# Kernel tuning notes

Hardware: AMD Instinct MI355X
Metric: run time of the kernel (lower is better)

## Reference

```python
import jax, jax.numpy as jnp
import numpy as np

N_M, N_C, D, H, E, EL = 200000, 50000, 128, 64, 1000000, 100000


def gat_conv(h_src, h_dst, W_src, W_dst, a_src, a_dst, b, src, dst, n_dst):
    # PyG GATConv (heads=1): project, per-edge attention logit, segment softmax over dst, weighted scatter-sum.
    hs = h_src @ W_src                      # [Ns, H]
    hd = h_dst @ W_dst                      # [Nd, H]
    al_s = hs @ a_src                       # [Ns]
    al_d = hd @ a_dst                       # [Nd]
    alpha = jax.nn.leaky_relu(al_s[src] + al_d[dst], 0.2)   # [E]
    m = jax.ops.segment_max(alpha, dst, num_segments=n_dst)
    m = jnp.where(jnp.isfinite(m), m, 0.0)
    e = jnp.exp(alpha - m[dst])
    denom = jax.ops.segment_sum(e, dst, num_segments=n_dst)
    w = e / jnp.maximum(denom[dst], 1e-16)
    out = jax.ops.segment_sum(w[:, None] * hs[src], dst, num_segments=n_dst)
    return out + b


def setup_inputs() -> dict:
    key = jax.random.key(0)
    ks = jax.random.split(key, 32)
    p = lambda k, s: (jax.random.normal(k, s, jnp.float32) * 0.1)
    inp = {
        'x_m': jax.random.normal(ks[0], (N_M, D), jnp.float32),
        'x_c': jax.random.normal(ks[1], (N_C, D), jnp.float32),
        'src_mc': jax.random.randint(ks[2], (E,), 0, N_M, jnp.int32),
        'dst_mc': jax.random.randint(ks[3], (E,), 0, N_C, jnp.int32),
        'src_cm': jax.random.randint(ks[4], (E,), 0, N_C, jnp.int32),
        'dst_cm': jax.random.randint(ks[5], (E,), 0, N_M, jnp.int32),
        'row': jax.random.randint(ks[6], (EL,), 0, N_M, jnp.int32),
        'col': jax.random.randint(ks[7], (EL,), 0, N_C, jnp.int32),
        'W1s_mc': p(ks[8], (D, H)), 'W1d_mc': p(ks[9], (D, H)),
        'a1s_mc': p(ks[10], (H,)), 'a1d_mc': p(ks[11], (H,)), 'b1_mc': p(ks[12], (H,)),
        'W1s_cm': p(ks[13], (D, H)), 'W1d_cm': p(ks[14], (D, H)),
        'a1s_cm': p(ks[15], (H,)), 'a1d_cm': p(ks[16], (H,)), 'b1_cm': p(ks[17], (H,)),
        'W2s_mc': p(ks[18], (H, H)), 'W2d_mc': p(ks[19], (H, H)),
        'a2s_mc': p(ks[20], (H,)), 'a2d_mc': p(ks[21], (H,)), 'b2_mc': p(ks[22], (H,)),
        'W2s_cm': p(ks[23], (H, H)), 'W2d_cm': p(ks[24], (H, H)),
        'a2s_cm': p(ks[25], (H,)), 'a2d_cm': p(ks[26], (H,)), 'b2_cm': p(ks[27], (H,)),
        'Wd1': p(ks[28], (2 * H, H)), 'bd1': p(ks[29], (H,)),
        'Wd2': p(ks[30], (H, 2)), 'bd2': p(ks[31], (2,)),
    }
    return inp


def reference(x_m, x_c, src_mc, dst_mc, src_cm, dst_cm, row, col,
              W1s_mc, W1d_mc, a1s_mc, a1d_mc, b1_mc,
              W1s_cm, W1d_cm, a1s_cm, a1d_cm, b1_cm,
              W2s_mc, W2d_mc, a2s_mc, a2d_mc, b2_mc,
              W2s_cm, W2d_cm, a2s_cm, a2d_cm, b2_cm,
              Wd1, bd1, Wd2, bd2):
    # Layer 1: materials receive only via concepts->materials edges; concepts via materials->concepts.
    z_c = jax.nn.relu(gat_conv(x_m, x_c, W1s_mc, W1d_mc, a1s_mc, a1d_mc, b1_mc, src_mc, dst_mc, N_C))
    z_m = jax.nn.relu(gat_conv(x_c, x_m, W1s_cm, W1d_cm, a1s_cm, a1d_cm, b1_cm, src_cm, dst_cm, N_M))
    # Layer 2 (no activation)
    z_c2 = gat_conv(z_m, z_c, W2s_mc, W2d_mc, a2s_mc, a2d_mc, b2_mc, src_mc, dst_mc, N_C)
    z_m2 = gat_conv(z_c, z_m, W2s_cm, W2d_cm, a2s_cm, a2d_cm, b2_cm, src_cm, dst_cm, N_M)
    # Edge decoder: gather-concat + 2-layer MLP (no activation between, per source)
    z = jnp.concatenate([z_m2[row], z_c2[col]], axis=-1)   # [EL, 2H]
    z = z @ Wd1 + bd1
    z = z @ Wd2 + bd2
    return z.reshape(-1)
```

## Files before the change

### kernel.cpp

```cpp
#include <hip/hip_runtime.h>
#include <hip/hip_fp16.h>
#include <cstdint>
#include <cstddef>

typedef _Float16 f16x8 __attribute__((ext_vector_type(8)));
typedef float f32x4 __attribute__((ext_vector_type(4)));

__device__ __forceinline__ float exp_am8(float a) {
    return __builtin_amdgcn_exp2f(fmaf(a, 1.442695040888963f, -11.541560327111707f));
}

__global__ __launch_bounds__(256) void bucket_hist(const int* __restrict__ dA,
                                                   int* __restrict__ bcntA, int shA,
                                                   const int* __restrict__ dB,
                                                   int* __restrict__ bcntB, int shB,
                                                   int E, int nblkA) {
    __shared__ int h[256];
    const int* dst; int* bcnt; int sh; int base;
    if ((int)blockIdx.x < nblkA) { dst = dA; bcnt = bcntA; sh = shA; base = blockIdx.x * 4096; }
    else { dst = dB; bcnt = bcntB; sh = shB; base = (blockIdx.x - nblkA) * 4096; }
    int t = threadIdx.x;
    h[t] = 0;
    __syncthreads();
#pragma unroll
    for (int j = 0; j < 16; ++j) {
        int i = base + j * 256 + t;
        if (i < E) atomicAdd(&h[dst[i] >> sh], 1);
    }
    __syncthreads();
    int c = h[t];
    if (c > 0) atomicAdd(&bcnt[t], c);
}

__global__ void bucket_scan(const int* __restrict__ bcntA, int nbkA,
                            int* __restrict__ bbaseA, int* __restrict__ bcurA,
                            int* __restrict__ offA, int nA,
                            const int* __restrict__ bcntB, int nbkB,
                            int* __restrict__ bbaseB, int* __restrict__ bcurB,
                            int* __restrict__ offB, int nB, int E) {
    int t = threadIdx.x;
    if (t == 0) {
        int run = 0;
        for (int i = 0; i < nbkA; ++i) { bbaseA[i] = run; bcurA[i] = run; run += bcntA[i]; }
        bbaseA[nbkA] = run;
        offA[nA] = E;
    }
    if (t == 64) {
        int run = 0;
        for (int i = 0; i < nbkB; ++i) { bbaseB[i] = run; bcurB[i] = run; run += bcntB[i]; }
        bbaseB[nbkB] = run;
        offB[nB] = E;
    }
}

__global__ __launch_bounds__(256) void bucket_scatter(
    const int* __restrict__ srcA, const int* __restrict__ dstA,
    int* __restrict__ bcurA, unsigned* __restrict__ pairsA,
    const int* __restrict__ srcB, const int* __restrict__ dstB,
    int* __restrict__ bcurB, unsigned* __restrict__ pairsB,
    int E, int nblkA, int shA, int shB, int srcbits) {
    __shared__ int bcnt[256];
    __shared__ int bbase[256];
    const int* src; const int* dst; int* bcur; unsigned* pairs; int sh; int base;
    if ((int)blockIdx.x < nblkA) {
        src = srcA; dst = dstA; bcur = bcurA; pairs = pairsA; sh = shA;
        base = blockIdx.x * 4096;
    } else {
        src = srcB; dst = dstB; bcur = bcurB; pairs = pairsB; sh = shB;
        base = (blockIdx.x - nblkA) * 4096;
    }
    int t = threadIdx.x;
    int msk = (1 << sh) - 1;
    bcnt[t] = 0;
    __syncthreads();
    int sreg[16], dreg[16];
#pragma unroll
    for (int j = 0; j < 16; ++j) {
        int i = base + j * 256 + t;
        if (i < E) {
            sreg[j] = src[i];
            dreg[j] = dst[i];
            atomicAdd(&bcnt[dreg[j] >> sh], 1);
        } else {
            dreg[j] = -1;
        }
    }
    __syncthreads();
    {
        int c = bcnt[t];
        int g = (c > 0) ? atomicAdd(&bcur[t], c) : 0;
        bbase[t] = g;
        bcnt[t] = 0;
    }
    __syncthreads();
#pragma unroll
    for (int j = 0; j < 16; ++j) {
        if (dreg[j] >= 0) {
            int b = dreg[j] >> sh;
            int r = atomicAdd(&bcnt[b], 1);
            pairs[bbase[b] + r] = ((unsigned)(dreg[j] & msk) << srcbits) | (unsigned)sreg[j];
        }
    }
}

__global__ __launch_bounds__(256) void bucket_expand2(
    const unsigned* __restrict__ pairsA, const int* __restrict__ bbaseA, int nA,
    int* __restrict__ offA, int* __restrict__ csrA, int shA, int nbA,
    const unsigned* __restrict__ pairsB, const int* __restrict__ bbaseB, int nB,
    int* __restrict__ offB, int* __restrict__ csrB, int shB, int srcbits) {
    __shared__ int lcnt[1024];
    __shared__ int red[256];
    const unsigned* pairs; const int* bbase; int n; int* off; int* csr; int sh; int b;
    if ((int)blockIdx.x < nbA) {
        pairs = pairsA; bbase = bbaseA; n = nA; off = offA; csr = csrA; sh = shA;
        b = blockIdx.x;
    } else {
        pairs = pairsB; bbase = bbaseB; n = nB; off = offB; csr = csrB; sh = shB;
        b = blockIdx.x - nbA;
    }
    int dpb = 1 << sh;
    int d0 = b << sh;
    int t = threadIdx.x;
    unsigned smask = (1u << srcbits) - 1u;
    for (int dl = t; dl < dpb; dl += 256) lcnt[dl] = 0;
    __syncthreads();
    int pbeg = bbase[b], pend = bbase[b + 1];
    for (int i = pbeg + t; i < pend; i += 256)
        atomicAdd(&lcnt[pairs[i] >> srcbits], 1);
    __syncthreads();
    int per = (dpb + 255) >> 8;
    int i0 = t * per;
    int s = 0;
    for (int j = 0; j < per; ++j) {
        int dl = i0 + j;
        if (dl < dpb) s += lcnt[dl];
    }
    red[t] = s;
    __syncthreads();
    for (int st = 1; st < 256; st <<= 1) {
        int tmp = (t >= st) ? red[t - st] : 0;
        __syncthreads();
        red[t] += tmp;
        __syncthreads();
    }
    int run = pbeg + red[t] - s;
    for (int j = 0; j < per; ++j) {
        int dl = i0 + j;
        if (dl < dpb) {
            int c = lcnt[dl];
            if (d0 + dl < n) off[d0 + dl] = run;
            lcnt[dl] = run;
            run += c;
        }
    }
    __syncthreads();
    for (int i = pbeg + t; i < pend; i += 256) {
        unsigned p = pairs[i];
        int dl = (int)(p >> srcbits);
        int pos = atomicAdd(&lcnt[dl], 1);
        csr[pos] = (int)(p & smask);
    }
}

__global__ __launch_bounds__(256) void pack_w2(
    const float* __restrict__ Wa0, const float* __restrict__ Wb0, _Float16* __restrict__ P0,
    const float* __restrict__ Wa1, const float* __restrict__ Wb1, _Float16* __restrict__ P1) {
    int b = blockIdx.x;
    const float* Wa; const float* Wb; _Float16* Wp; int lb;
    if (b < 64) { Wa = Wa0; Wb = Wb0; Wp = P0; lb = b; }
    else        { Wa = Wa1; Wb = Wb1; Wp = P1; lb = b - 64; }
    constexpr int K = 128;
    constexpr int NKB = K / 32;
    int i = lb * 256 + threadIdx.x;
    if (i >= 128 * K) return;
    int k = i >> 7, c = i & 127;
    float v = (c < 64) ? Wa[k * 64 + c] : Wb[k * 64 + (c - 64)];
    int ct = c >> 4, lr = c & 15, kb = k >> 5, lk = (k & 31) >> 3, e = k & 7;
    Wp[((ct * NKB + kb) * 64 + (lr + 16 * lk)) * 8 + e] = (_Float16)v;
}

__global__ void decoder_prep3(const float* __restrict__ Wd1, const float* __restrict__ bd1,
                              const float* __restrict__ Wd2, const float* __restrict__ bd2,
                              const float* __restrict__ b2_cm, const float* __restrict__ b2_mc,
                              const float* __restrict__ W2s_mc, const float* __restrict__ a2s_mc,
                              const float* __restrict__ W2d_cm, const float* __restrict__ a2d_cm,
                              const float* __restrict__ W2s_cm, const float* __restrict__ a2s_cm,
                              const float* __restrict__ W2d_mc, const float* __restrict__ a2d_mc,
                              float* __restrict__ Wc, float* __restrict__ bc,
                              float* __restrict__ bq,
                              float4* __restrict__ foldA, float4* __restrict__ foldB) {
    __shared__ float WcS[256];
    int t = threadIdx.x;
    int k = t >> 1, c = t & 1;
    float s = 0.f;
    for (int j = 0; j < 64; ++j) s += Wd1[k * 64 + j] * Wd2[j * 2 + c];
    Wc[k * 2 + c] = s;
    WcS[k * 2 + c] = s;
    if (k == 0) {
        float b = bd2[c];
        for (int j = 0; j < 64; ++j) b += bd1[j] * Wd2[j * 2 + c];
        bc[c] = b;
    }
    __syncthreads();
    if (t < 2) {
        float v = 0.f;
        for (int j = 0; j < 64; ++j) v += b2_cm[j] * WcS[j * 2 + t];
        bq[t] = v;
    } else if (t < 4) {
        int cc = t - 2;
        float v = 0.f;
        for (int j = 0; j < 64; ++j) v += b2_mc[j] * WcS[(64 + j) * 2 + cc];
        bq[t] = v;
    }
    if (t < 64) {
        int j = t;
        float fa = 0.f, fd = 0.f, qx = 0.f, qy = 0.f;
        for (int cc = 0; cc < 64; ++cc) {
            float ws = W2s_mc[j * 64 + cc];
            fa += ws * a2s_mc[cc];
            qx += ws * WcS[(64 + cc) * 2 + 0];
            qy += ws * WcS[(64 + cc) * 2 + 1];
            fd += W2d_cm[j * 64 + cc] * a2d_cm[cc];
        }
        foldA[j] = make_float4(fa, fd, qx, qy);
    } else if (t < 128) {
        int j = t - 64;
        float fa = 0.f, fd = 0.f, qx = 0.f, qy = 0.f;
        for (int cc = 0; cc < 64; ++cc) {
            float ws = W2s_cm[j * 64 + cc];
            fa += ws * a2s_cm[cc];
            qx += ws * WcS[cc * 2 + 0];
            qy += ws * WcS[cc * 2 + 1];
            fd += W2d_mc[j * 64 + cc] * a2d_mc[cc];
        }
        foldB[j] = make_float4(fa, fd, qx, qy);
    }
}

template <int K>
__global__ __launch_bounds__(256) void proj_mfma3_kernel(const float* __restrict__ X, int N,
                                                         const _Float16* __restrict__ Wp,
                                                         const float* __restrict__ a0v,
                                                         const float* __restrict__ a1v,
                                                         __half* __restrict__ out0,
                                                         float* __restrict__ al0,
                                                         float* __restrict__ al1) {
    constexpr int NKB = K / 32;
    __shared__ __align__(16) _Float16 Wlds[128 * K];
    int t = threadIdx.x;
    constexpr int NV = (128 * K) / 8;
#pragma unroll
    for (int i = t; i < NV; i += 256)
        ((uint4*)Wlds)[i] = ((const uint4*)Wp)[i];
    __syncthreads();

    int rt = blockIdx.x * 64;
    int wv = t >> 6, lane = t & 63, lr = lane & 15, lk = lane >> 4;
    int row = rt + wv * 16 + lr;
    int rowc = row < N ? row : N - 1;

    f32x4 acc[8];
#pragma unroll
    for (int i = 0; i < 8; ++i) acc[i] = f32x4{0.f, 0.f, 0.f, 0.f};

    const f16x8* Wf = (const f16x8*)Wlds;
#pragma unroll
    for (int kb = 0; kb < NKB; ++kb) {
        f16x8 bf;
        const float* xr = X + (size_t)rowc * K + kb * 32 + lk * 8;
        float4 x0 = *(const float4*)xr;
        float4 x1 = *(const float4*)(xr + 4);
        bf[0] = (_Float16)x0.x; bf[1] = (_Float16)x0.y;
        bf[2] = (_Float16)x0.z; bf[3] = (_Float16)x0.w;
        bf[4] = (_Float16)x1.x; bf[5] = (_Float16)x1.y;
        bf[6] = (_Float16)x1.z; bf[7] = (_Float16)x1.w;
#pragma unroll
        for (int ct = 0; ct < 8; ++ct) {
            acc[ct] = __builtin_amdgcn_mfma_f32_16x16x32_f16(Wf[(ct * NKB + kb) * 64 + lane],
                                                             bf, acc[ct], 0, 0, 0);
        }
    }

    float p0 = 0.f, p1 = 0.f;
#pragma unroll
    for (int ct = 0; ct < 4; ++ct) {
        float4 aq = ((const float4*)a0v)[ct * 4 + lk];
        f32x4 v = acc[ct];
        p0 += v[0] * aq.x + v[1] * aq.y + v[2] * aq.z + v[3] * aq.w;
    }
#pragma unroll
    for (int ct = 0; ct < 4; ++ct) {
        float4 aq = ((const float4*)a1v)[ct * 4 + lk];
        f32x4 v = acc[4 + ct];
        p1 += v[0] * aq.x + v[1] * aq.y + v[2] * aq.z + v[3] * aq.w;
    }
    p0 += __shfl_xor(p0, 16); p0 += __shfl_xor(p0, 32);
    p1 += __shfl_xor(p1, 16); p1 += __shfl_xor(p1, 32);
    if (row < N) {
#pragma unroll
        for (int ct = 0; ct < 4; ++ct) {
            f32x4 v = acc[ct];
            __half2 h01 = __floats2half2_rn(v[0], v[1]);
            __half2 h23 = __floats2half2_rn(v[2], v[3]);
            uint2 pk;
            pk.x = *(const unsigned int*)&h01;
            pk.y = *(const unsigned int*)&h23;
            *(uint2*)(out0 + ((size_t)row << 6) + ct * 16 + lk * 4) = pk;
        }
        if (lane < 16) { al0[row] = p0; al1[row] = p1; }
    }
}

#define AGG_CAP 64
#define AGG_PAD 66

__global__ __launch_bounds__(256) void gat_aggregate9f(
    const int* __restrict__ off0, const int* __restrict__ csr0,
    const __half* __restrict__ hs0, const float* __restrict__ als0,
    const float* __restrict__ ald0, const float* __restrict__ bias0,
    const float4* __restrict__ fold0, float* __restrict__ als2_0,
    float* __restrict__ ald2_0, float2* __restrict__ q2_0, int n0,
    const int* __restrict__ off1, const int* __restrict__ csr1,
    const __half* __restrict__ hs1, const float* __restrict__ als1,
    const float* __restrict__ ald1, const float* __restrict__ bias1,
    const float4* __restrict__ fold1, float* __restrict__ als2_1,
    float* __restrict__ ald2_1, float2* __restrict__ q2_1, int n1,
    int nb0) {
    __shared__ uint2 wP[16][AGG_PAD];
    int t = threadIdx.x;
    int slot = t >> 4;
    int sub = t & 15;

    const int* off; const int* csr; const __half* hs; const float* als;
    const float* ald; const float* bias; const float4* fold;
    float* als2; float* ald2; float2* q2; int nd; int b;
    if (blockIdx.x < (unsigned)nb0) {
        b = blockIdx.x;
        off = off0; csr = csr0; hs = hs0; als = als0; ald = ald0; bias = bias0;
        fold = fold0; als2 = als2_0; ald2 = ald2_0; q2 = q2_0; nd = n0;
    } else {
        b = blockIdx.x - nb0;
        off = off1; csr = csr1; hs = hs1; als = als1; ald = ald1; bias = bias1;
        fold = fold1; als2 = als2_1; ald2 = ald2_1; q2 = q2_1; nd = n1;
    }
    int d = b * 16 + slot;
    bool active = d < nd;
    int beg = 0, deg = 0;
    float aldv = 0.f;
    if (active) {
        beg = off[d];
        deg = off[d + 1] - beg;
        aldv = ald[d];
    }
    float4 bl4 = ((const float4*)bias)[sub];
    uint2* WP = wP[slot];

    float sum = 0.f;
    for (int i = sub; i < deg; i += 16) {
        int s = csr[beg + i];
        float a = als[s] + aldv;
        a = (a >= 0.f) ? a : 0.2f * a;
        float w = exp_am8(a);
        sum += w;
        if (i < AGG_CAP) {
            __half hw = __float2half_rn(w);
            __half2 h2 = __half2half2(hw);
            WP[i] = make_uint2(*(const unsigned int*)&h2, (unsigned int)s);
        }
    }
    sum += __shfl_xor(sum, 1);
    sum += __shfl_xor(sum, 2);
    sum += __shfl_xor(sum, 4);
    sum += __shfl_xor(sum, 8);
    float inv = 1.f / fmaxf(sum, 1e-16f);

    int dc = deg < AGG_CAP ? deg : AGG_CAP;
    const uint2* hs4 = (const uint2*)hs;
    __half2 z = __floats2half2_rn(0.f, 0.f);
    __half2 aA = z, aB = z, aC = z, aD = z;
    int i = 0;
    for (; i + 8 <= dc; i += 8) {
        uint4 q0 = *(const uint4*)&WP[i];
        uint4 q1 = *(const uint4*)&WP[i + 2];
        uint4 q2r = *(const uint4*)&WP[i + 4];
        uint4 q3 = *(const uint4*)&WP[i + 6];
        uint2 v0 = hs4[(size_t)q0.y * 16 + sub];
        uint2 v1 = hs4[(size_t)q0.w * 16 + sub];
        uint2 v2 = hs4[(size_t)q1.y * 16 + sub];
        uint2 v3 = hs4[(size_t)q1.w * 16 + sub];
        uint2 v4 = hs4[(size_t)q2r.y * 16 + sub];
        uint2 v5 = hs4[(size_t)q2r.w * 16 + sub];
        uint2 v6 = hs4[(size_t)q3.y * 16 + sub];
        uint2 v7 = hs4[(size_t)q3.w * 16 + sub];
        aA = __hfma2(*(const __half2*)&q0.x, *(const __half2*)&v0.x, aA);
        aB = __hfma2(*(const __half2*)&q0.x, *(const __half2*)&v0.y, aB);
        aC = __hfma2(*(const __half2*)&q0.z, *(const __half2*)&v1.x, aC);
        aD = __hfma2(*(const __half2*)&q0.z, *(const __half2*)&v1.y, aD);
        aA = __hfma2(*(const __half2*)&q1.x, *(const __half2*)&v2.x, aA);
        aB = __hfma2(*(const __half2*)&q1.x, *(const __half2*)&v2.y, aB);
        aC = __hfma2(*(const __half2*)&q1.z, *(const __half2*)&v3.x, aC);
        aD = __hfma2(*(const __half2*)&q1.z, *(const __half2*)&v3.y, aD);
        aA = __hfma2(*(const __half2*)&q2r.x, *(const __half2*)&v4.x, aA);
        aB = __hfma2(*(const __half2*)&q2r.x, *(const __half2*)&v4.y, aB);
        aC = __hfma2(*(const __half2*)&q2r.z, *(const __half2*)&v5.x, aC);
        aD = __hfma2(*(const __half2*)&q2r.z, *(const __half2*)&v5.y, aD);
        aA = __hfma2(*(const __half2*)&q3.x, *(const __half2*)&v6.x, aA);
        aB = __hfma2(*(const __half2*)&q3.x, *(const __half2*)&v6.y, aB);
        aC = __hfma2(*(const __half2*)&q3.z, *(const __half2*)&v7.x, aC);
        aD = __hfma2(*(const __half2*)&q3.z, *(const __half2*)&v7.y, aD);
    }
    for (; i + 2 <= dc; i += 2) {
        uint4 q = *(const uint4*)&WP[i];
        uint2 v0 = hs4[(size_t)q.y * 16 + sub];
        uint2 v1 = hs4[(size_t)q.w * 16 + sub];
        aA = __hfma2(*(const __half2*)&q.x, *(const __half2*)&v0.x, aA);
        aB = __hfma2(*(const __half2*)&q.x, *(const __half2*)&v0.y, aB);
        aC = __hfma2(*(const __half2*)&q.z, *(const __half2*)&v1.x, aC);
        aD = __hfma2(*(const __half2*)&q.z, *(const __half2*)&v1.y, aD);
    }
    if (i < dc) {
        uint2 u = WP[i];
        uint2 v = hs4[(size_t)u.y * 16 + sub];
        aA = __hfma2(*(const __half2*)&u.x, *(const __half2*)&v.x, aA);
        aB = __hfma2(*(const __half2*)&u.x, *(const __half2*)&v.y, aB);
    }
    for (int j = AGG_CAP; j < deg; ++j) {
        int s = csr[beg + j];
        float a = als[s] + aldv;
        a = (a >= 0.f) ? a : 0.2f * a;
        __half hw = __float2half_rn(exp_am8(a));
        __half2 w2 = __half2half2(hw);
        uint2 v = hs4[(size_t)s * 16 + sub];
        aA = __hfma2(w2, *(const __half2*)&v.x, aA);
        aB = __hfma2(w2, *(const __half2*)&v.y, aB);
    }
    float2 fA = __half22float2(aA);
    float2 fB = __half22float2(aB);
    float2 fC = __half22float2(aC);
    float2 fD = __half22float2(aD);
    float o0 = (fA.x + fC.x) * inv + bl4.x;
    float o1 = (fA.y + fC.y) * inv + bl4.y;
    float o2 = (fB.x + fD.x) * inv + bl4.z;
    float o3 = (fB.y + fD.y) * inv + bl4.w;
    if (deg == 0) { o0 = bl4.x; o1 = bl4.y; o2 = bl4.z; o3 = bl4.w; }
    o0 = fmaxf(o0, 0.f); o1 = fmaxf(o1, 0.f);
    o2 = fmaxf(o2, 0.f); o3 = fmaxf(o3, 0.f);

    float4 f0 = fold[4 * sub + 0];
    float4 f1 = fold[4 * sub + 1];
    float4 f2 = fold[4 * sub + 2];
    float4 f3 = fold[4 * sub + 3];
    float a0 = o0 * f0.x + o1 * f1.x + o2 * f2.x + o3 * f3.x;
    float a1 = o0 * f0.y + o1 * f1.y + o2 * f2.y + o3 * f3.y;
    float a2 = o0 * f0.z + o1 * f1.z + o2 * f2.z + o3 * f3.z;
    float a3 = o0 * f0.w + o1 * f1.w + o2 * f2.w + o3 * f3.w;
#pragma unroll
    for (int o = 1; o < 16; o <<= 1) {
        a0 += __shfl_xor(a0, o);
        a1 += __shfl_xor(a1, o);
        a2 += __shfl_xor(a2, o);
        a3 += __shfl_xor(a3, o);
    }
    if (active && sub == 0) {
        als2[d] = a0;
        ald2[d] = a1;
        q2[d] = make_float2(a2, a3);
    }
}

__global__ __launch_bounds__(256) void gat_aggregate10p(
    const int* __restrict__ off0, const int* __restrict__ csr0,
    const float2* __restrict__ q0, const float* __restrict__ als0,
    const float* __restrict__ ald0, const float2* __restrict__ bqp,
    float2* __restrict__ out0, int n0,
    const int* __restrict__ off1, const int* __restrict__ csr1,
    const float2* __restrict__ q1, const float* __restrict__ als1,
    const float* __restrict__ ald1,
    float2* __restrict__ out1, int n1,
    int nb0) {
    const int* off; const int* csr; const float2* qt; const float* als;
    const float* ald; float2 bq; float2* outp; int nd; int b;
    if (blockIdx.x < (unsigned)nb0) {
        b = blockIdx.x;
        off = off0; csr = csr0; qt = q0; als = als0; ald = ald0; bq = bqp[1];
        outp = out0; nd = n0;
    } else {
        b = blockIdx.x - nb0;
        off = off1; csr = csr1; qt = q1; als = als1; ald = ald1; bq = bqp[0];
        outp = out1; nd = n1;
    }
    int d = b * 256 + threadIdx.x;
    if (d >= nd) return;
    int beg = off[d], end = off[d + 1];
    float aldv = ald[d];
    float sum = 0.f, ax = 0.f, ay = 0.f;
    int i = beg;
    for (; i + 2 <= end; i += 2) {
        int s0 = csr[i], s1 = csr[i + 1];
        float a0 = als[s0] + aldv;
        float a1 = als[s1] + aldv;
        float2 v0 = qt[s0];
        float2 v1 = qt[s1];
        a0 = (a0 >= 0.f) ? a0 : 0.2f * a0;
        a1 = (a1 >= 0.f) ? a1 : 0.2f * a1;
        float w0 = exp_am8(a0);
        float w1 = exp_am8(a1);
        sum += w0 + w1;
        ax = fmaf(w0, v0.x, ax); ay = fmaf(w0, v0.y, ay);
        ax = fmaf(w1, v1.x, ax); ay = fmaf(w1, v1.y, ay);
    }
    if (i < end) {
        int s = csr[i];
        float a = als[s] + aldv;
        a = (a >= 0.f) ? a : 0.2f * a;
        float w = exp_am8(a);
        float2 v = qt[s];
        sum += w;
        ax = fmaf(w, v.x, ax); ay = fmaf(w, v.y, ay);
    }
    float inv = 1.f / fmaxf(sum, 1e-16f);
    outp[d] = make_float2(ax * inv + bq.x, ay * inv + bq.y);
}

__global__ __launch_bounds__(256) void decoder4_kernel(const int* __restrict__ row,
                                                       const int* __restrict__ col,
                                                       const float2* __restrict__ pm,
                                                       const float2* __restrict__ pc,
                                                       const float* __restrict__ bc,
                                                       float* __restrict__ out, int EL) {
    int e = blockIdx.x * 256 + threadIdx.x;
    if (e >= EL) return;
    float2 a = pm[row[e]];
    float2 b = pc[col[e]];
    *(float2*)(out + 2 * (size_t)e) = make_float2(a.x + b.x + bc[0], a.y + b.y + bc[1]);
}

extern "C" void kernel_launch(void* const* d_in, const int* in_sizes, int n_in,
                              void* d_out, int out_size, void* d_ws, size_t ws_size,
                              hipStream_t stream) {
    const int D = 128;
    const float* x_m    = (const float*)d_in[0];
    const float* x_c    = (const float*)d_in[1];
    const int*   src_mc = (const int*)d_in[2];
    const int*   dst_mc = (const int*)d_in[3];
    const int*   src_cm = (const int*)d_in[4];
    const int*   dst_cm = (const int*)d_in[5];
    const int*   rowi   = (const int*)d_in[6];
    const int*   coli   = (const int*)d_in[7];
    const float* W1s_mc = (const float*)d_in[8];
    const float* W1d_mc = (const float*)d_in[9];
    const float* a1s_mc = (const float*)d_in[10];
    const float* a1d_mc = (const float*)d_in[11];
    const float* b1_mc  = (const float*)d_in[12];
    const float* W1s_cm = (const float*)d_in[13];
    const float* W1d_cm = (const float*)d_in[14];
    const float* a1s_cm = (const float*)d_in[15];
    const float* a1d_cm = (const float*)d_in[16];
    const float* b1_cm  = (const float*)d_in[17];
    const float* W2s_mc = (const float*)d_in[18];
    const float* W2d_mc = (const float*)d_in[19];
    const float* a2s_mc = (const float*)d_in[20];
    const float* a2d_mc = (const float*)d_in[21];
    const float* b2_mc  = (const float*)d_in[22];
    const float* W2s_cm = (const float*)d_in[23];
    const float* W2d_cm = (const float*)d_in[24];
    const float* a2s_cm = (const float*)d_in[25];
    const float* a2d_cm = (const float*)d_in[26];
    const float* b2_cm  = (const float*)d_in[27];
    const float* Wd1    = (const float*)d_in[28];
    const float* bd1    = (const float*)d_in[29];
    const float* Wd2    = (const float*)d_in[30];
    const float* bd2    = (const float*)d_in[31];

    const int N_M = in_sizes[0] / D;
    const int N_C = in_sizes[1] / D;
    const int E   = in_sizes[2];
    const int EL  = in_sizes[6];
    float* out = (float*)d_out;

    uint8_t* base = (uint8_t*)d_ws;
    size_t off = 0;
    auto carve = [&](size_t bytes) -> void* {
        void* p = base + off;
        off += (bytes + 255) & ~(size_t)255;
        return p;
    };
    __half* hsA_h = (__half*)carve((size_t)N_M * 64 * 2);
    __half* hsB_h = (__half*)carve((size_t)N_C * 64 * 2);
    float2* qA    = (float2*)carve((size_t)N_M * 8);
    float2* qB    = (float2*)carve((size_t)N_C * 8);
    float2* pm_m  = (float2*)carve((size_t)N_M * 8);
    float2* pm_c  = (float2*)carve((size_t)N_C * 8);
    float* als_mc = (float*)carve((size_t)N_M * 4);
    float* ald_cm = (float*)carve((size_t)N_M * 4);
    float* als_cm = (float*)carve((size_t)N_C * 4);
    float* ald_mc = (float*)carve((size_t)N_C * 4);
    float* als2_mc = (float*)carve((size_t)N_M * 4);
    float* ald2_cm = (float*)carve((size_t)N_M * 4);
    float* als2_cm = (float*)carve((size_t)N_C * 4);
    float* ald2_mc = (float*)carve((size_t)N_C * 4);
    int* off_mc = (int*)carve((size_t)(N_C + 1) * 4);
    int* off_cm = (int*)carve((size_t)(N_M + 1) * 4);
    int* csr_mc = (int*)carve((size_t)E * 4);
    int* csr_cm = (int*)carve((size_t)E * 4);
    unsigned* pairs_mc = (unsigned*)carve((size_t)E * 4);
    unsigned* pairs_cm = (unsigned*)carve((size_t)E * 4);
    int* bcnt_base = (int*)carve(512 * 4);
    int* bcnt_mc = bcnt_base;
    int* bcnt_cm = bcnt_base + 256;
    int* bbase_mc = (int*)carve(257 * 4);
    int* bbase_cm = (int*)carve(257 * 4);
    int* bcur_mc = (int*)carve(256 * 4);
    int* bcur_cm = (int*)carve(256 * 4);
    _Float16* wp1A = (_Float16*)carve(128 * 128 * 2);
    _Float16* wp1B = (_Float16*)carve(128 * 128 * 2);
    float* Wc = (float*)carve(256 * 4);
    float* bc = (float*)carve(256);
    float* bq = (float*)carve(256);
    float2* bq2 = (float2*)bq;
    float4* foldA = (float4*)carve(64 * 16);
    float4* foldB = (float4*)carve(64 * 16);

    int shA = 0; while (((N_C + (1 << shA) - 1) >> shA) > 256) shA++;
    int shB = 0; while (((N_M + (1 << shB) - 1) >> shB) > 256) shB++;
    int nbkA = (N_C + (1 << shA) - 1) >> shA;
    int nbkB = (N_M + (1 << shB) - 1) >> shB;
    int maxN = N_M > N_C ? N_M : N_C;
    int srcbits = 1; while ((1 << srcbits) < maxN) srcbits++;

    pack_w2<<<128, 256, 0, stream>>>(W1s_mc, W1d_cm, wp1A, W1s_cm, W1d_mc, wp1B);
    decoder_prep3<<<1, 256, 0, stream>>>(Wd1, bd1, Wd2, bd2, b2_cm, b2_mc,
                                         W2s_mc, a2s_mc, W2d_cm, a2d_cm,
                                         W2s_cm, a2s_cm, W2d_mc, a2d_mc,
                                         Wc, bc, bq, foldA, foldB);

    hipMemsetAsync(bcnt_base, 0, 512 * 4, stream);
    int nblk = (E + 4095) / 4096;
    bucket_hist<<<2 * nblk, 256, 0, stream>>>(dst_mc, bcnt_mc, shA,
                                              dst_cm, bcnt_cm, shB, E, nblk);
    bucket_scan<<<1, 128, 0, stream>>>(bcnt_mc, nbkA, bbase_mc, bcur_mc, off_mc, N_C,
                                       bcnt_cm, nbkB, bbase_cm, bcur_cm, off_cm, N_M, E);
    bucket_scatter<<<2 * nblk, 256, 0, stream>>>(
        src_mc, dst_mc, bcur_mc, pairs_mc,
        src_cm, dst_cm, bcur_cm, pairs_cm, E, nblk, shA, shB, srcbits);
    bucket_expand2<<<nbkA + nbkB, 256, 0, stream>>>(
        pairs_mc, bbase_mc, N_C, off_mc, csr_mc, shA, nbkA,
        pairs_cm, bbase_cm, N_M, off_cm, csr_cm, shB, srcbits);

    int nb_c16 = (N_C + 15) / 16;
    int nb_m16 = (N_M + 15) / 16;

    proj_mfma3_kernel<128><<<(N_M + 63) / 64, 256, 0, stream>>>(
        x_m, N_M, wp1A, a1s_mc, a1d_cm, hsA_h, als_mc, ald_cm);
    proj_mfma3_kernel<128><<<(N_C + 63) / 64, 256, 0, stream>>>(
        x_c, N_C, wp1B, a1s_cm, a1d_mc, hsB_h, als_cm, ald_mc);
    gat_aggregate9f<<<nb_c16 + nb_m16, 256, 0, stream>>>(
        off_mc, csr_mc, hsA_h, als_mc, ald_mc, b1_mc, foldB, als2_cm, ald2_mc, qB, N_C,
        off_cm, csr_cm, hsB_h, als_cm, ald_cm, b1_cm, foldA, als2_mc, ald2_cm, qA, N_M,
        nb_c16);

    int nb_c256 = (N_C + 255) / 256;
    int nb_m256 = (N_M + 255) / 256;
    gat_aggregate10p<<<nb_c256 + nb_m256, 256, 0, stream>>>(
        off_mc, csr_mc, qA, als2_mc, ald2_mc, bq2, pm_c, N_C,
        off_cm, csr_cm, qB, als2_cm, ald2_cm, pm_m, N_M, nb_c256);

    decoder4_kernel<<<(EL + 255) / 256, 256, 0, stream>>>(rowi, coli, pm_m, pm_c, bc, out, EL);
}
```

Measured before the change: 214.5 us.

## Merge prep kernels and fuse layer-1 projections with bucket histogram launch

Combines weight packing, decoder folding and the histogram-counter zeroing into one prep kernel, replacing two launches and a memset. Merges both layer-1 MFMA projections and the destination bucket histogram into a single heterogeneous launch with dynamic shared memory. This cuts launch count and lets projection work overlap with histogram work. In exchange, the histogram blocks now reserve 32KB of LDS, which can lower their occupancy, and the projections now run before the CSR build.

```diff
diff --git a/kernel.cpp b/kernel.cpp
--- a/kernel.cpp
+++ b/kernel.cpp
@@ -10,15 +10,184 @@
     return __builtin_amdgcn_exp2f(fmaf(a, 1.442695040888963f, -11.541560327111707f));
 }
 
-__global__ __launch_bounds__(256) void bucket_hist(const int* __restrict__ dA,
-                                                   int* __restrict__ bcntA, int shA,
-                                                   const int* __restrict__ dB,
-                                                   int* __restrict__ bcntB, int shB,
-                                                   int E, int nblkA) {
-    __shared__ int h[256];
+__global__ void prep_all(
+    const float* __restrict__ Wa0, const float* __restrict__ Wb0, _Float16* __restrict__ P0,
+    const float* __restrict__ Wa1, const float* __restrict__ Wb1, _Float16* __restrict__ P1,
+    const float* __restrict__ Wd1, const float* __restrict__ bd1,
+    const float* __restrict__ Wd2, const float* __restrict__ bd2,
+    const float* __restrict__ b2_cm, const float* __restrict__ b2_mc,
+    const float* __restrict__ W2s_mc, const float* __restrict__ a2s_mc,
+    const float* __restrict__ W2d_cm, const float* __restrict__ a2d_cm,
+    const float* __restrict__ W2s_cm, const float* __restrict__ a2s_cm,
+    const float* __restrict__ W2d_mc, const float* __restrict__ a2d_mc,
+    float* __restrict__ Wc, float* __restrict__ bc, float* __restrict__ bq,
+    float4* __restrict__ foldA, float4* __restrict__ foldB,
+    int* __restrict__ bcnt_base) {
+    __shared__ float WcS[256];
+    int b = blockIdx.x;
+    int t = threadIdx.x;
+    if (b < 128) {
+        const float* Wa; const float* Wb; _Float16* Wp; int lb;
+        if (b < 64) { Wa = Wa0; Wb = Wb0; Wp = P0; lb = b; }
+        else        { Wa = Wa1; Wb = Wb1; Wp = P1; lb = b - 64; }
+        constexpr int K = 128;
+        constexpr int NKB = K / 32;
+        int i = lb * 256 + t;
+        if (i >= 128 * K) return;
+        int k = i >> 7, c = i & 127;
+        float v = (c < 64) ? Wa[k * 64 + c] : Wb[k * 64 + (c - 64)];
+        int ct = c >> 4, lr = c & 15, kb = k >> 5, lk = (k & 31) >> 3, e = k & 7;
+        Wp[((ct * NKB + kb) * 64 + (lr + 16 * lk)) * 8 + e] = (_Float16)v;
+    } else if (b == 128) {
+        int k = t >> 1, c = t & 1;
+        float s = 0.f;
+        for (int j = 0; j < 64; ++j) s += Wd1[k * 64 + j] * Wd2[j * 2 + c];
+        Wc[k * 2 + c] = s;
+        WcS[k * 2 + c] = s;
+        if (k == 0) {
+            float bv = bd2[c];
+            for (int j = 0; j < 64; ++j) bv += bd1[j] * Wd2[j * 2 + c];
+            bc[c] = bv;
+        }
+        __syncthreads();
+        if (t < 2) {
+            float v = 0.f;
+            for (int j = 0; j < 64; ++j) v += b2_cm[j] * WcS[j * 2 + t];
+            bq[t] = v;
+        } else if (t < 4) {
+            int cc = t - 2;
+            float v = 0.f;
+            for (int j = 0; j < 64; ++j) v += b2_mc[j] * WcS[(64 + j) * 2 + cc];
+            bq[t] = v;
+        }
+        if (t < 64) {
+            int j = t;
+            float fa = 0.f, fd = 0.f, qx = 0.f, qy = 0.f;
+            for (int cc = 0; cc < 64; ++cc) {
+                float ws = W2s_mc[j * 64 + cc];
+                fa += ws * a2s_mc[cc];
+                qx += ws * WcS[(64 + cc) * 2 + 0];
+                qy += ws * WcS[(64 + cc) * 2 + 1];
+                fd += W2d_cm[j * 64 + cc] * a2d_cm[cc];
+            }
+            foldA[j] = make_float4(fa, fd, qx, qy);
+        } else if (t < 128) {
+            int j = t - 64;
+            float fa = 0.f, fd = 0.f, qx = 0.f, qy = 0.f;
+            for (int cc = 0; cc < 64; ++cc) {
+                float ws = W2s_cm[j * 64 + cc];
+                fa += ws * a2s_cm[cc];
+                qx += ws * WcS[cc * 2 + 0];
+                qy += ws * WcS[cc * 2 + 1];
+                fd += W2d_mc[j * 64 + cc] * a2d_mc[cc];
+            }
+            foldB[j] = make_float4(fa, fd, qx, qy);
+        }
+    } else {
+        bcnt_base[t] = 0;
+        bcnt_base[t + 256] = 0;
+    }
+}
+
+__device__ __forceinline__ void proj_body(const float* __restrict__ X, int N,
+                                          const _Float16* __restrict__ Wp,
+                                          const float* __restrict__ a0v,
+                                          const float* __restrict__ a1v,
+                                          __half* __restrict__ out0,
+                                          float* __restrict__ al0,
+                                          float* __restrict__ al1,
+                                          _Float16* Wlds, int blk) {
+    constexpr int K = 128;
+    constexpr int NKB = K / 32;
+    int t = threadIdx.x;
+    constexpr int NV = (128 * K) / 8;
+#pragma unroll
+    for (int i = t; i < NV; i += 256)
+        ((uint4*)Wlds)[i] = ((const uint4*)Wp)[i];
+    __syncthreads();
+
+    int rt = blk * 64;
+    int wv = t >> 6, lane = t & 63, lr = lane & 15, lk = lane >> 4;
+    int row = rt + wv * 16 + lr;
+    int rowc = row < N ? row : N - 1;
+
+    f32x4 acc[8];
+#pragma unroll
+    for (int i = 0; i < 8; ++i) acc[i] = f32x4{0.f, 0.f, 0.f, 0.f};
+
+    const f16x8* Wf = (const f16x8*)Wlds;
+#pragma unroll
+    for (int kb = 0; kb < NKB; ++kb) {
+        f16x8 bf;
+        const float* xr = X + (size_t)rowc * K + kb * 32 + lk * 8;
+        float4 x0 = *(const float4*)xr;
+        float4 x1 = *(const float4*)(xr + 4);
+        bf[0] = (_Float16)x0.x; bf[1] = (_Float16)x0.y;
+        bf[2] = (_Float16)x0.z; bf[3] = (_Float16)x0.w;
+        bf[4] = (_Float16)x1.x; bf[5] = (_Float16)x1.y;
+        bf[6] = (_Float16)x1.z; bf[7] = (_Float16)x1.w;
+#pragma unroll
+        for (int ct = 0; ct < 8; ++ct) {
+            acc[ct] = __builtin_amdgcn_mfma_f32_16x16x32_f16(Wf[(ct * NKB + kb) * 64 + lane],
+                                                             bf, acc[ct], 0, 0, 0);
+        }
+    }
+
+    float p0 = 0.f, p1 = 0.f;
+#pragma unroll
+    for (int ct = 0; ct < 4; ++ct) {
+        float4 aq = ((const float4*)a0v)[ct * 4 + lk];
+        f32x4 v = acc[ct];
+        p0 += v[0] * aq.x + v[1] * aq.y + v[2] * aq.z + v[3] * aq.w;
+    }
+#pragma unroll
+    for (int ct = 0; ct < 4; ++ct) {
+        float4 aq = ((const float4*)a1v)[ct * 4 + lk];
+        f32x4 v = acc[4 + ct];
+        p1 += v[0] * aq.x + v[1] * aq.y + v[2] * aq.z + v[3] * aq.w;
+    }
+    p0 += __shfl_xor(p0, 16); p0 += __shfl_xor(p0, 32);
+    p1 += __shfl_xor(p1, 16); p1 += __shfl_xor(p1, 32);
+    if (row < N) {
+#pragma unroll
+        for (int ct = 0; ct < 4; ++ct) {
+            f32x4 v = acc[ct];
+            __half2 h01 = __floats2half2_rn(v[0], v[1]);
+            __half2 h23 = __floats2half2_rn(v[2], v[3]);
+            uint2 pk;
+            pk.x = *(const unsigned int*)&h01;
+            pk.y = *(const unsigned int*)&h23;
+            *(uint2*)(out0 + ((size_t)row << 6) + ct * 16 + lk * 4) = pk;
+        }
+        if (lane < 16) { al0[row] = p0; al1[row] = p1; }
+    }
+}
+
+__global__ __launch_bounds__(256) void fused_proj_hist(
+    const float* __restrict__ Xm, int Nm, const _Float16* __restrict__ WpA,
+    const float* __restrict__ a0A, const float* __restrict__ a1A,
+    __half* __restrict__ outA, float* __restrict__ al0A, float* __restrict__ al1A, int nbm,
+    const float* __restrict__ Xc, int Nc, const _Float16* __restrict__ WpB,
+    const float* __restrict__ a0B, const float* __restrict__ a1B,
+    __half* __restrict__ outB, float* __restrict__ al0B, float* __restrict__ al1B, int nbc,
+    const int* __restrict__ dmc, int* __restrict__ bcnt_mc, int shA,
+    const int* __restrict__ dcm, int* __restrict__ bcnt_cm, int shB, int E, int nblk) {
+    extern __shared__ __align__(16) char smem[];
+    int b = blockIdx.x;
+    if (b < nbm) {
+        proj_body(Xm, Nm, WpA, a0A, a1A, outA, al0A, al1A, (_Float16*)smem, b);
+        return;
+    }
+    b -= nbm;
+    if (b < nbc) {
+        proj_body(Xc, Nc, WpB, a0B, a1B, outB, al0B, al1B, (_Float16*)smem, b);
+        return;
+    }
+    b -= nbc;
+    int* h = (int*)smem;
     const int* dst; int* bcnt; int sh; int base;
-    if ((int)blockIdx.x < nblkA) { dst = dA; bcnt = bcntA; sh = shA; base = blockIdx.x * 4096; }
-    else { dst = dB; bcnt = bcntB; sh = shB; base = (blockIdx.x - nblkA) * 4096; }
+    if (b < nblk) { dst = dmc; bcnt = bcnt_mc; sh = shA; base = b * 4096; }
+    else { dst = dcm; bcnt = bcnt_cm; sh = shB; base = (b - nblk) * 4096; }
     int t = threadIdx.x;
     h[t] = 0;
     __syncthreads();
@@ -159,155 +328,6 @@
         int dl = (int)(p >> srcbits);
         int pos = atomicAdd(&lcnt[dl], 1);
         csr[pos] = (int)(p & smask);
-    }
-}
-
-__global__ __launch_bounds__(256) void pack_w2(
-    const float* __restrict__ Wa0, const float* __restrict__ Wb0, _Float16* __restrict__ P0,
-    const float* __restrict__ Wa1, const float* __restrict__ Wb1, _Float16* __restrict__ P1) {
-    int b = blockIdx.x;
-    const float* Wa; const float* Wb; _Float16* Wp; int lb;
-    if (b < 64) { Wa = Wa0; Wb = Wb0; Wp = P0; lb = b; }
-    else        { Wa = Wa1; Wb = Wb1; Wp = P1; lb = b - 64; }
-    constexpr int K = 128;
-    constexpr int NKB = K / 32;
-    int i = lb * 256 + threadIdx.x;
-    if (i >= 128 * K) return;
-    int k = i >> 7, c = i & 127;
-    float v = (c < 64) ? Wa[k * 64 + c] : Wb[k * 64 + (c - 64)];
-    int ct = c >> 4, lr = c & 15, kb = k >> 5, lk = (k & 31) >> 3, e = k & 7;
-    Wp[((ct * NKB + kb) * 64 + (lr + 16 * lk)) * 8 + e] = (_Float16)v;
-}
-
-__global__ void decoder_prep3(const float* __restrict__ Wd1, const float* __restrict__ bd1,
-                              const float* __restrict__ Wd2, const float* __restrict__ bd2,
-                              const float* __restrict__ b2_cm, const float* __restrict__ b2_mc,
-                              const float* __restrict__ W2s_mc, const float* __restrict__ a2s_mc,
-                              const float* __restrict__ W2d_cm, const float* __restrict__ a2d_cm,
-                              const float* __restrict__ W2s_cm, const float* __restrict__ a2s_cm,
-                              const float* __restrict__ W2d_mc, const float* __restrict__ a2d_mc,
-                              float* __restrict__ Wc, float* __restrict__ bc,
-                              float* __restrict__ bq,
-                              float4* __restrict__ foldA, float4* __restrict__ foldB) {
-    __shared__ float WcS[256];
-    int t = threadIdx.x;
-    int k = t >> 1, c = t & 1;
-    float s = 0.f;
-    for (int j = 0; j < 64; ++j) s += Wd1[k * 64 + j] * Wd2[j * 2 + c];
-    Wc[k * 2 + c] = s;
-    WcS[k * 2 + c] = s;
-    if (k == 0) {
-        float b = bd2[c];
-        for (int j = 0; j < 64; ++j) b += bd1[j] * Wd2[j * 2 + c];
-        bc[c] = b;
-    }
-    __syncthreads();
-    if (t < 2) {
-        float v = 0.f;
-        for (int j = 0; j < 64; ++j) v += b2_cm[j] * WcS[j * 2 + t];
-        bq[t] = v;
-    } else if (t < 4) {
-        int cc = t - 2;
-        float v = 0.f;
-        for (int j = 0; j < 64; ++j) v += b2_mc[j] * WcS[(64 + j) * 2 + cc];
-        bq[t] = v;
-    }
-    if (t < 64) {
-        int j = t;
-        float fa = 0.f, fd = 0.f, qx = 0.f, qy = 0.f;
-        for (int cc = 0; cc < 64; ++cc) {
-            float ws = W2s_mc[j * 64 + cc];
-            fa += ws * a2s_mc[cc];
-            qx += ws * WcS[(64 + cc) * 2 + 0];
-            qy += ws * WcS[(64 + cc) * 2 + 1];
-            fd += W2d_cm[j * 64 + cc] * a2d_cm[cc];
-        }
-        foldA[j] = make_float4(fa, fd, qx, qy);
-    } else if (t < 128) {
-        int j = t - 64;
-        float fa = 0.f, fd = 0.f, qx = 0.f, qy = 0.f;
-        for (int cc = 0; cc < 64; ++cc) {
-            float ws = W2s_cm[j * 64 + cc];
-            fa += ws * a2s_cm[cc];
-            qx += ws * WcS[cc * 2 + 0];
-            qy += ws * WcS[cc * 2 + 1];
-            fd += W2d_mc[j * 64 + cc] * a2d_mc[cc];
-        }
-        foldB[j] = make_float4(fa, fd, qx, qy);
-    }
-}
-
-template <int K>
-__global__ __launch_bounds__(256) void proj_mfma3_kernel(const float* __restrict__ X, int N,
-                                                         const _Float16* __restrict__ Wp,
-                                                         const float* __restrict__ a0v,
-                                                         const float* __restrict__ a1v,
-                                                         __half* __restrict__ out0,
-                                                         float* __restrict__ al0,
-                                                         float* __restrict__ al1) {
-    constexpr int NKB = K / 32;
-    __shared__ __align__(16) _Float16 Wlds[128 * K];
-    int t = threadIdx.x;
-    constexpr int NV = (128 * K) / 8;
-#pragma unroll
-    for (int i = t; i < NV; i += 256)
-        ((uint4*)Wlds)[i] = ((const uint4*)Wp)[i];
-    __syncthreads();
-
-    int rt = blockIdx.x * 64;
-    int wv = t >> 6, lane = t & 63, lr = lane & 15, lk = lane >> 4;
-    int row = rt + wv * 16 + lr;
-    int rowc = row < N ? row : N - 1;
-
-    f32x4 acc[8];
-#pragma unroll
-    for (int i = 0; i < 8; ++i) acc[i] = f32x4{0.f, 0.f, 0.f, 0.f};
-
-    const f16x8* Wf = (const f16x8*)Wlds;
-#pragma unroll
-    for (int kb = 0; kb < NKB; ++kb) {
-        f16x8 bf;
-        const float* xr = X + (size_t)rowc * K + kb * 32 + lk * 8;
-        float4 x0 = *(const float4*)xr;
-        float4 x1 = *(const float4*)(xr + 4);
-        bf[0] = (_Float16)x0.x; bf[1] = (_Float16)x0.y;
-        bf[2] = (_Float16)x0.z; bf[3] = (_Float16)x0.w;
-        bf[4] = (_Float16)x1.x; bf[5] = (_Float16)x1.y;
-        bf[6] = (_Float16)x1.z; bf[7] = (_Float16)x1.w;
-#pragma unroll
-        for (int ct = 0; ct < 8; ++ct) {
-            acc[ct] = __builtin_amdgcn_mfma_f32_16x16x32_f16(Wf[(ct * NKB + kb) * 64 + lane],
-                                                             bf, acc[ct], 0, 0, 0);
-        }
-    }
-
-    float p0 = 0.f, p1 = 0.f;
-#pragma unroll
-    for (int ct = 0; ct < 4; ++ct) {
-        float4 aq = ((const float4*)a0v)[ct * 4 + lk];
-        f32x4 v = acc[ct];
-        p0 += v[0] * aq.x + v[1] * aq.y + v[2] * aq.z + v[3] * aq.w;
-    }
-#pragma unroll
-    for (int ct = 0; ct < 4; ++ct) {
-        float4 aq = ((const float4*)a1v)[ct * 4 + lk];
-        f32x4 v = acc[4 + ct];
-        p1 += v[0] * aq.x + v[1] * aq.y + v[2] * aq.z + v[3] * aq.w;
-    }
-    p0 += __shfl_xor(p0, 16); p0 += __shfl_xor(p0, 32);
-    p1 += __shfl_xor(p1, 16); p1 += __shfl_xor(p1, 32);
-    if (row < N) {
-#pragma unroll
-        for (int ct = 0; ct < 4; ++ct) {
-            f32x4 v = acc[ct];
-            __half2 h01 = __floats2half2_rn(v[0], v[1]);
-            __half2 h23 = __floats2half2_rn(v[2], v[3]);
-            uint2 pk;
-            pk.x = *(const unsigned int*)&h01;
-            pk.y = *(const unsigned int*)&h23;
-            *(uint2*)(out0 + ((size_t)row << 6) + ct * 16 + lk * 4) = pk;
-        }
-        if (lane < 16) { al0[row] = p0; al1[row] = p1; }
     }
 }
 
@@ -628,16 +648,20 @@
     int maxN = N_M > N_C ? N_M : N_C;
     int srcbits = 1; while ((1 << srcbits) < maxN) srcbits++;
 
-    pack_w2<<<128, 256, 0, stream>>>(W1s_mc, W1d_cm, wp1A, W1s_cm, W1d_mc, wp1B);
-    decoder_prep3<<<1, 256, 0, stream>>>(Wd1, bd1, Wd2, bd2, b2_cm, b2_mc,
-                                         W2s_mc, a2s_mc, W2d_cm, a2d_cm,
-                                         W2s_cm, a2s_cm, W2d_mc, a2d_mc,
-                                         Wc, bc, bq, foldA, foldB);
-
-    hipMemsetAsync(bcnt_base, 0, 512 * 4, stream);
+    prep_all<<<130, 256, 0, stream>>>(W1s_mc, W1d_cm, wp1A, W1s_cm, W1d_mc, wp1B,
+                                      Wd1, bd1, Wd2, bd2, b2_cm, b2_mc,
+                                      W2s_mc, a2s_mc, W2d_cm, a2d_cm,
+                                      W2s_cm, a2s_cm, W2d_mc, a2d_mc,
+                                      Wc, bc, bq, foldA, foldB, bcnt_base);
+
+    int nbm = (N_M + 63) / 64;
+    int nbc = (N_C + 63) / 64;
     int nblk = (E + 4095) / 4096;
-    bucket_hist<<<2 * nblk, 256, 0, stream>>>(dst_mc, bcnt_mc, shA,
-                                              dst_cm, bcnt_cm, shB, E, nblk);
+    fused_proj_hist<<<nbm + nbc + 2 * nblk, 256, 32768, stream>>>(
+        x_m, N_M, wp1A, a1s_mc, a1d_cm, hsA_h, als_mc, ald_cm, nbm,
+        x_c, N_C, wp1B, a1s_cm, a1d_mc, hsB_h, als_cm, ald_mc, nbc,
+        dst_mc, bcnt_mc, shA, dst_cm, bcnt_cm, shB, E, nblk);
+
     bucket_scan<<<1, 128, 0, stream>>>(bcnt_mc, nbkA, bbase_mc, bcur_mc, off_mc, N_C,
                                        bcnt_cm, nbkB, bbase_cm, bcur_cm, off_cm, N_M, E);
     bucket_scatter<<<2 * nblk, 256, 0, stream>>>(
@@ -650,10 +674,6 @@
     int nb_c16 = (N_C + 15) / 16;
     int nb_m16 = (N_M + 15) / 16;
 
-    proj_mfma3_kernel<128><<<(N_M + 63) / 64, 256, 0, stream>>>(
-        x_m, N_M, wp1A, a1s_mc, a1d_cm, hsA_h, als_mc, ald_cm);
-    proj_mfma3_kernel<128><<<(N_C + 63) / 64, 256, 0, stream>>>(
-        x_c, N_C, wp1B, a1s_cm, a1d_mc, hsB_h, als_cm, ald_mc);
     gat_aggregate9f<<<nb_c16 + nb_m16, 256, 0, stream>>>(
         off_mc, csr_mc, hsA_h, als_mc, ald_mc, b1_mc, foldB, als2_cm, ald2_mc, qB, N_C,
         off_cm, csr_cm, hsB_h, als_cm, ald_cm, b1_cm, foldA, als2_mc, ald2_cm, qA, N_M,
```

Result: faster. 199.7 us (-6.9%).
